# Kernel tuning notes

Measured on AMD Instinct MI355X. Metric: run time of the kernel, lower is better.

The kernel has to match this reference:

```python
import jax, jax.numpy as jnp
import numpy as np

LN_EPS = 1e-5


def setup_inputs() -> dict:
    key = jax.random.key(0)
    ks = jax.random.split(key, 6)
    B, S, D = 4, 4096, 2048
    Db = D // 4  # bottleneck_dim = n_embd // compression_ratio
    hidden = jax.random.normal(ks[0], (B, S, D), dtype=jnp.float32)
    # LayerNorm params (torch defaults: gamma=1, beta=0)
    ln_gamma = jnp.ones((D,), dtype=jnp.float32)
    ln_beta = jnp.zeros((D,), dtype=jnp.float32)
    # Linear weights, torch default init: U(-1/sqrt(fan_in), 1/sqrt(fan_in))
    bd_lim = 1.0 / np.sqrt(D)
    W_down = jax.random.uniform(ks[1], (D, Db), minval=-bd_lim, maxval=bd_lim, dtype=jnp.float32)
    b_down = jax.random.uniform(ks[2], (Db,), minval=-bd_lim, maxval=bd_lim, dtype=jnp.float32)
    bu_lim = 1.0 / np.sqrt(Db)
    W_up = jax.random.uniform(ks[3], (Db, D), minval=-bu_lim, maxval=bu_lim, dtype=jnp.float32)
    b_up = jax.random.uniform(ks[4], (D,), minval=-bu_lim, maxval=bu_lim, dtype=jnp.float32)
    alpha = jnp.array(0.01, dtype=jnp.float32)
    return {
        "hidden": hidden,
        "ln_gamma": ln_gamma,
        "ln_beta": ln_beta,
        "W_down": W_down,
        "b_down": b_down,
        "W_up": W_up,
        "b_up": b_up,
        "alpha": alpha,
        "layer_idx": 0,
    }


def reference(hidden, ln_gamma, ln_beta, W_down, b_down, W_up, b_up, alpha, layer_idx):
    # LayerNorm over last dim
    mu = jnp.mean(hidden, axis=-1, keepdims=True)
    var = jnp.mean(jnp.square(hidden - mu), axis=-1, keepdims=True)
    h_norm = (hidden - mu) * jax.lax.rsqrt(var + LN_EPS) * ln_gamma + ln_beta
    # down-proj -> SiLU -> up-proj   [b s d] @ [d k] -> [b s k] -> [b s d]
    z = jnp.einsum("bsd,dk->bsk", h_norm, W_down) + b_down
    z = jax.nn.silu(z)
    bottleneck_out = jnp.einsum("bsk,kd->bsd", z, W_up) + b_up
    # alpha-gated residual
    return hidden + alpha * (bottleneck_out - hidden)
```

## Files before the change

### kernel.cpp

```cpp
#include <hip/hip_runtime.h>

typedef __bf16 bf16x8 __attribute__((ext_vector_type(8)));
typedef __bf16 bf16x4 __attribute__((ext_vector_type(4)));
typedef float f32x4 __attribute__((ext_vector_type(4)));

#define S_BARRIER() asm volatile("s_barrier" ::: "memory")
#define WAITCNT_VM(n) asm volatile("s_waitcnt vmcnt(" #n ")" ::: "memory")
#define WAITCNT_LGKM0() asm volatile("s_waitcnt lgkmcnt(0)" ::: "memory")

__global__ __launch_bounds__(256) void prep_w_kernel(
    const float* __restrict__ Wd, __bf16* __restrict__ Wtd,
    const float* __restrict__ Wu, __bf16* __restrict__ Wtu,
    const float* __restrict__ g, const float* __restrict__ be,
    float* __restrict__ C1, float* __restrict__ C2b,
    int D, int Db) {
    const int ntile_d = (Db / 32) * (D / 32);
    __shared__ float t[32][33];
    const int c = threadIdx.x & 31, r0 = threadIdx.x >> 5;
    if ((int)blockIdx.x < ntile_d) {
        const int K = D, N = Db, tile = blockIdx.x;
        const int tn = tile % (N / 32), tk = tile / (N / 32);
        const int n0 = tn * 32, k0 = tk * 32;
#pragma unroll
        for (int r = r0; r < 32; r += 8)
            t[r][c] = Wd[(size_t)(k0 + r) * N + n0 + c];
        __syncthreads();
        const float gv = g[k0 + c];
        const float bv = be[k0 + c];
        float c1p[4], c2p[4];
#pragma unroll
        for (int u = 0; u < 4; ++u) {
            const int r = r0 + u * 8;
            const float wv = t[c][r];
            const __bf16 w16 = (__bf16)(gv * wv);
            Wtd[(size_t)(n0 + r) * K + k0 + c] = w16;
            c1p[u] = (float)w16;
            c2p[u] = bv * wv;
        }
#pragma unroll
        for (int o = 16; o > 0; o >>= 1)
#pragma unroll
            for (int u = 0; u < 4; ++u) {
                c1p[u] += __shfl_xor(c1p[u], o);
                c2p[u] += __shfl_xor(c2p[u], o);
            }
        if (c == 0)
#pragma unroll
            for (int u = 0; u < 4; ++u) {
                atomicAdd(&C1[n0 + r0 + u * 8], c1p[u]);
                atomicAdd(&C2b[n0 + r0 + u * 8], c2p[u]);
            }
    } else {
        const int K = Db, N = D, tile = blockIdx.x - ntile_d;
        const int tn = tile % (N / 32), tk = tile / (N / 32);
        const int n0 = tn * 32, k0 = tk * 32;
#pragma unroll
        for (int r = r0; r < 32; r += 8)
            t[r][c] = Wu[(size_t)(k0 + r) * N + n0 + c];
        __syncthreads();
#pragma unroll
        for (int r = r0; r < 32; r += 8)
            Wtu[(size_t)(n0 + r) * K + k0 + c] = (__bf16)t[c][r];
    }
}

__global__ __launch_bounds__(256, 4) void fused_ln_down(
    const float* __restrict__ X, const __bf16* __restrict__ Bt,
    const float* __restrict__ C1, const float* __restrict__ C2b,
    __bf16* __restrict__ Z, int M, int N, int K) {
    constexpr int BM = 64, BN = 128, BK = 32;
    constexpr int WM = 32, WN = 64, MI = 2, NJ = 4;
    __shared__ __align__(16) __bf16 Ads[BM * BK];
    __shared__ __align__(16) __bf16 Bds[2][BN * BK];
    __shared__ float sRow[BM], ssRow[BM];

    const int tid = threadIdx.x;
    const int wave = tid >> 6, lane = tid & 63;
    const int bn = blockIdx.x, bm = blockIdx.y;
    const int row0 = bm * BM, col0 = bn * BN;
    const int wr = wave >> 1, wc = wave & 1;

    f32x4 acc[MI][NJ] = {};

    const int lrow = lane >> 2;
    const int chunk = (lane & 3) ^ (lrow & 3);
    const int arow = wave * 16 + lrow;
    const float* Axr = X + (size_t)(row0 + arow) * K + chunk * 8;
    const __bf16* Bg = Bt + (size_t)col0 * K;
    const int lk = chunk * 8;

    const int c = lane & 15, q = lane >> 4;

    auto stageB = [&](int k0, int b) {
#pragma unroll
        for (int p = 0; p < 2; ++p) {
            const int r = wave * 32 + p * 16;
            __builtin_amdgcn_global_load_lds(
                (__attribute__((address_space(1))) void*)(Bg + (size_t)(r + lrow) * K + k0 + lk),
                (__attribute__((address_space(3))) void*)(&Bds[b][r * BK]),
                16, 0, 0);
        }
    };

    float s = 0.f, ss = 0.f;
    const int nk = K / BK;
    stageB(0, 0);
    float4 a0 = *(const float4*)(Axr);
    float4 a1 = *(const float4*)(Axr + 4);
    for (int it = 0; it < nk; ++it) {
        const int cur = it & 1;
        float4 n0, n1;
        if (it + 1 < nk) {
            stageB((it + 1) * BK, cur ^ 1);
            n0 = *(const float4*)(Axr + (it + 1) * BK);
            n1 = *(const float4*)(Axr + (it + 1) * BK + 4);
            WAITCNT_VM(4);
        } else {
            WAITCNT_VM(0);
        }
        s += a0.x + a0.y + a0.z + a0.w + a1.x + a1.y + a1.z + a1.w;
        ss += a0.x * a0.x + a0.y * a0.y + a0.z * a0.z + a0.w * a0.w +
              a1.x * a1.x + a1.y * a1.y + a1.z * a1.z + a1.w * a1.w;
        bf16x8 av;
        av[0] = (__bf16)a0.x; av[1] = (__bf16)a0.y;
        av[2] = (__bf16)a0.z; av[3] = (__bf16)a0.w;
        av[4] = (__bf16)a1.x; av[5] = (__bf16)a1.y;
        av[6] = (__bf16)a1.z; av[7] = (__bf16)a1.w;
        *(bf16x8*)(&Ads[arow * BK + (lane & 3) * 8]) = av;
        WAITCNT_LGKM0();
        S_BARRIER();

        bf16x8 afW[NJ], bfA[MI];
#pragma unroll
        for (int j = 0; j < NJ; ++j) {
            const int rl = wc * WN + j * 16 + c;
            afW[j] = *(const bf16x8*)(&Bds[cur][rl * BK + ((q ^ (c & 3)) * 8)]);
        }
#pragma unroll
        for (int i = 0; i < MI; ++i) {
            const int rl = wr * WM + i * 16 + c;
            bfA[i] = *(const bf16x8*)(&Ads[rl * BK + ((q ^ (c & 3)) * 8)]);
        }
#pragma unroll
        for (int i = 0; i < MI; ++i)
#pragma unroll
            for (int j = 0; j < NJ; ++j)
                acc[i][j] = __builtin_amdgcn_mfma_f32_16x16x32_bf16(afW[j], bfA[i],
                                                                    acc[i][j], 0, 0, 0);
        WAITCNT_LGKM0();
        S_BARRIER();
        a0 = n0; a1 = n1;
    }

    s += __shfl_xor(s, 1);  s += __shfl_xor(s, 2);
    ss += __shfl_xor(ss, 1); ss += __shfl_xor(ss, 2);
    if ((lane & 3) == 0) { sRow[arow] = s; ssRow[arow] = ss; }
    __syncthreads();

    const float rK = 1.f / (float)K;
#pragma unroll
    for (int i = 0; i < MI; ++i) {
        const int rl = wr * WM + i * 16 + c;
        const float mu = sRow[rl] * rK;
        const float var = ssRow[rl] * rK - mu * mu;
        const float rstd = rsqrtf(var + 1e-5f);
        const float mrs = mu * rstd;
        const int rowg = row0 + rl;
#pragma unroll
        for (int j = 0; j < NJ; ++j) {
            const int colb = col0 + wc * WN + j * 16 + q * 4;
            const float4 c1 = *(const float4*)(C1 + colb);
            const float4 c2 = *(const float4*)(C2b + colb);
            float v0 = rstd * acc[i][j][0] - mrs * c1.x + c2.x;
            float v1 = rstd * acc[i][j][1] - mrs * c1.y + c2.y;
            float v2 = rstd * acc[i][j][2] - mrs * c1.z + c2.z;
            float v3 = rstd * acc[i][j][3] - mrs * c1.w + c2.w;
            bf16x4 o;
            o[0] = (__bf16)(v0 / (1.f + __expf(-v0)));
            o[1] = (__bf16)(v1 / (1.f + __expf(-v1)));
            o[2] = (__bf16)(v2 / (1.f + __expf(-v2)));
            o[3] = (__bf16)(v3 / (1.f + __expf(-v3)));
            *(bf16x4*)(Z + (size_t)rowg * N + colb) = o;
        }
    }
}

template <int EPI, int BM, int BN, int MINW>
__global__ __launch_bounds__(256, MINW) void gemm_bt(
    const __bf16* __restrict__ A, const __bf16* __restrict__ Bt,
    const float* __restrict__ bias, const float* __restrict__ hid,
    const float* __restrict__ alpha_p, void* __restrict__ Cout,
    int M, int N, int K) {
    constexpr int BK = 32;
    constexpr int WM = BM / 2, WN = BN / 2;
    constexpr int MI = WM / 16, NJ = WN / 16;
    constexpr int GA = BM / 64, GB = BN / 64;
    constexpr int L = GA + GB;
    __shared__ __align__(16) __bf16 Ads[2][BM * BK];
    __shared__ __align__(16) __bf16 Bds[2][BN * BK];

    const int tid = threadIdx.x;
    const int wave = tid >> 6;
    const int lane = tid & 63;
    const int bn = blockIdx.x, bm = blockIdx.y;
    const int row0 = bm * BM, col0 = bn * BN;
    const int wr = wave >> 1, wc = wave & 1;

    f32x4 acc[MI][NJ] = {};

    const __bf16* Ag = A + (size_t)row0 * K;
    const __bf16* Bg = Bt + (size_t)col0 * K;
    const int lrow = lane >> 2;
    const int lk = ((lane & 3) ^ (lrow & 3)) * 8;

    const int c = lane & 15;
    const int q = lane >> 4;

    auto stage = [&](int k0, int b) {
#pragma unroll
        for (int p = 0; p < GA; ++p) {
            const int r = wave * (16 * GA) + p * 16;
            __builtin_amdgcn_global_load_lds(
                (__attribute__((address_space(1))) void*)(Ag + (size_t)(r + lrow) * K + k0 + lk),
                (__attribute__((address_space(3))) void*)(&Ads[b][r * BK]),
                16, 0, 0);
        }
#pragma unroll
        for (int p = 0; p < GB; ++p) {
            const int r = wave * (16 * GB) + p * 16;
            __builtin_amdgcn_global_load_lds(
                (__attribute__((address_space(1))) void*)(Bg + (size_t)(r + lrow) * K + k0 + lk),
                (__attribute__((address_space(3))) void*)(&Bds[b][r * BK]),
                16, 0, 0);
        }
    };

    const int nk = K / BK;
    stage(0, 0);
    for (int it = 0; it < nk; ++it) {
        const int cur = it & 1;
        if (it + 1 < nk) {
            stage((it + 1) * BK, cur ^ 1);
            if constexpr (L == 3) WAITCNT_VM(3); else WAITCNT_VM(4);
        } else {
            WAITCNT_VM(0);
        }
        S_BARRIER();

        bf16x8 afW[NJ], bfA[MI];
#pragma unroll
        for (int j = 0; j < NJ; ++j) {
            const int rl = wc * WN + j * 16 + c;
            afW[j] = *(const bf16x8*)(&Bds[cur][rl * BK + ((q ^ (c & 3)) * 8)]);
        }
#pragma unroll
        for (int i = 0; i < MI; ++i) {
            const int rl = wr * WM + i * 16 + c;
            bfA[i] = *(const bf16x8*)(&Ads[cur][rl * BK + ((q ^ (c & 3)) * 8)]);
        }
#pragma unroll
        for (int i = 0; i < MI; ++i)
#pragma unroll
            for (int j = 0; j < NJ; ++j)
                acc[i][j] = __builtin_amdgcn_mfma_f32_16x16x32_bf16(afW[j], bfA[i],
                                                                    acc[i][j], 0, 0, 0);
        WAITCNT_LGKM0();
        S_BARRIER();
    }

    float alpha = (EPI == 1) ? *alpha_p : 0.f;
#pragma unroll
    for (int i = 0; i < MI; ++i) {
        const int rowg = row0 + wr * WM + i * 16 + c;
        if (EPI == 0) {
#pragma unroll
            for (int j = 0; j < NJ; ++j) {
                const int colb = col0 + wc * WN + j * 16 + q * 4;
                const float4 bv = *(const float4*)(bias + colb);
                float v0 = acc[i][j][0] + bv.x;
                float v1 = acc[i][j][1] + bv.y;
                float v2 = acc[i][j][2] + bv.z;
                float v3 = acc[i][j][3] + bv.w;
                const size_t idx = (size_t)rowg * N + colb;
                bf16x4 o;
                o[0] = (__bf16)(v0 / (1.f + __expf(-v0)));
                o[1] = (__bf16)(v1 / (1.f + __expf(-v1)));
                o[2] = (__bf16)(v2 / (1.f + __expf(-v2)));
                o[3] = (__bf16)(v3 / (1.f + __expf(-v3)));
                *(bf16x4*)((__bf16*)Cout + idx) = o;
            }
        } else {
            float4 hv[NJ];
#pragma unroll
            for (int j = 0; j < NJ; ++j) {
                const int colb = col0 + wc * WN + j * 16 + q * 4;
                hv[j] = *(const float4*)(hid + (size_t)rowg * N + colb);
            }
#pragma unroll
            for (int j = 0; j < NJ; ++j) {
                const int colb = col0 + wc * WN + j * 16 + q * 4;
                const float4 bv = *(const float4*)(bias + colb);
                float v0 = acc[i][j][0] + bv.x;
                float v1 = acc[i][j][1] + bv.y;
                float v2 = acc[i][j][2] + bv.z;
                float v3 = acc[i][j][3] + bv.w;
                float4 o;
                o.x = hv[j].x + alpha * (v0 - hv[j].x);
                o.y = hv[j].y + alpha * (v1 - hv[j].y);
                o.z = hv[j].z + alpha * (v2 - hv[j].z);
                o.w = hv[j].w + alpha * (v3 - hv[j].w);
                *(float4*)((float*)Cout + (size_t)rowg * N + colb) = o;
            }
        }
    }
}

extern "C" void kernel_launch(void* const* d_in, const int* in_sizes, int n_in,
                              void* d_out, int out_size, void* d_ws, size_t ws_size,
                              hipStream_t stream) {
    const float* hidden = (const float*)d_in[0];
    const float* ln_gamma = (const float*)d_in[1];
    const float* ln_beta = (const float*)d_in[2];
    const float* W_down = (const float*)d_in[3];
    const float* b_down = (const float*)d_in[4];
    const float* W_up = (const float*)d_in[5];
    const float* b_up = (const float*)d_in[6];
    const float* alpha = (const float*)d_in[7];
    float* out = (float*)d_out;

    const int D = in_sizes[2];
    const int Db = in_sizes[4];
    const int M = in_sizes[0] / D;

    char* w = (char*)d_ws;
    __bf16* z = (__bf16*)w;   w += (size_t)M * Db * sizeof(__bf16);
    __bf16* Wtd = (__bf16*)w; w += (size_t)D * Db * sizeof(__bf16);
    __bf16* Wtu = (__bf16*)w; w += (size_t)Db * D * sizeof(__bf16);
    float* C1 = (float*)w;    w += Db * sizeof(float);
    float* C2b = (float*)w;   w += Db * sizeof(float);

    hipMemsetAsync(C1, 0, Db * sizeof(float), stream);
    hipMemcpyAsync(C2b, b_down, Db * sizeof(float), hipMemcpyDeviceToDevice, stream);

    const int ntiles = 2 * (D / 32) * (Db / 32);
    prep_w_kernel<<<ntiles, 256, 0, stream>>>(W_down, Wtd, W_up, Wtu,
                                              ln_gamma, ln_beta, C1, C2b, D, Db);

    fused_ln_down<<<dim3(Db / 128, M / 64), 256, 0, stream>>>(
        hidden, Wtd, C1, C2b, z, M, Db, D);

    gemm_bt<1, 128, 128, 4><<<dim3(D / 128, M / 128), 256, 0, stream>>>(
        z, Wtu, b_up, hidden, alpha, (void*)out, M, D, Db);
}
```

Measured before the change: 406.8 us.

## Deepen K tile to 64 in fused LN-down GEMM and add nontemporal memory ops

The fused LayerNorm+down-projection kernel now processes a 64-wide K slice per iteration, split into two 32-wide sub-buffers, so half as many barriers and loop iterations are needed and more loads are in flight per step. A-tile shared memory is double-buffered per sub-block, and the occupancy hint drops from 4 to 3 waves per SIMD to fit the larger LDS and register footprint. Streaming loads of hidden and stores of Z and the output use nontemporal builtins to reduce cache pollution. The cost is lower occupancy and more registers held for the prefetched A values.

```diff
diff --git a/kernel.cpp b/kernel.cpp
--- a/kernel.cpp
+++ b/kernel.cpp
@@ -64,14 +64,14 @@
     }
 }
 
-__global__ __launch_bounds__(256, 4) void fused_ln_down(
+__global__ __launch_bounds__(256, 3) void fused_ln_down(
     const float* __restrict__ X, const __bf16* __restrict__ Bt,
     const float* __restrict__ C1, const float* __restrict__ C2b,
     __bf16* __restrict__ Z, int M, int N, int K) {
-    constexpr int BM = 64, BN = 128, BK = 32;
+    constexpr int BM = 64, BN = 128, BK = 64;
     constexpr int WM = 32, WN = 64, MI = 2, NJ = 4;
-    __shared__ __align__(16) __bf16 Ads[BM * BK];
-    __shared__ __align__(16) __bf16 Bds[2][BN * BK];
+    __shared__ __align__(16) __bf16 Ads[2][BM * 32];
+    __shared__ __align__(16) __bf16 Bds[2][2][BN * 32];
     __shared__ float sRow[BM], ssRow[BM];
 
     const int tid = threadIdx.x;
@@ -95,61 +95,81 @@
 #pragma unroll
         for (int p = 0; p < 2; ++p) {
             const int r = wave * 32 + p * 16;
-            __builtin_amdgcn_global_load_lds(
-                (__attribute__((address_space(1))) void*)(Bg + (size_t)(r + lrow) * K + k0 + lk),
-                (__attribute__((address_space(3))) void*)(&Bds[b][r * BK]),
-                16, 0, 0);
+#pragma unroll
+            for (int kb = 0; kb < 2; ++kb) {
+                __builtin_amdgcn_global_load_lds(
+                    (__attribute__((address_space(1))) void*)(Bg + (size_t)(r + lrow) * K + k0 + kb * 32 + lk),
+                    (__attribute__((address_space(3))) void*)(&Bds[b][kb][r * 32]),
+                    16, 0, 0);
+            }
+        }
+    };
+
+    auto ldA = [&](int it, f32x4* d) {
+#pragma unroll
+        for (int kb = 0; kb < 2; ++kb) {
+            d[kb * 2] = __builtin_nontemporal_load((const f32x4*)(Axr + it * BK + kb * 32));
+            d[kb * 2 + 1] = __builtin_nontemporal_load((const f32x4*)(Axr + it * BK + kb * 32 + 4));
         }
     };
 
     float s = 0.f, ss = 0.f;
     const int nk = K / BK;
     stageB(0, 0);
-    float4 a0 = *(const float4*)(Axr);
-    float4 a1 = *(const float4*)(Axr + 4);
+    f32x4 a[4];
+    ldA(0, a);
     for (int it = 0; it < nk; ++it) {
         const int cur = it & 1;
-        float4 n0, n1;
+        f32x4 nx[4];
         if (it + 1 < nk) {
             stageB((it + 1) * BK, cur ^ 1);
-            n0 = *(const float4*)(Axr + (it + 1) * BK);
-            n1 = *(const float4*)(Axr + (it + 1) * BK + 4);
-            WAITCNT_VM(4);
+            ldA(it + 1, nx);
+            WAITCNT_VM(8);
         } else {
             WAITCNT_VM(0);
         }
-        s += a0.x + a0.y + a0.z + a0.w + a1.x + a1.y + a1.z + a1.w;
-        ss += a0.x * a0.x + a0.y * a0.y + a0.z * a0.z + a0.w * a0.w +
-              a1.x * a1.x + a1.y * a1.y + a1.z * a1.z + a1.w * a1.w;
-        bf16x8 av;
-        av[0] = (__bf16)a0.x; av[1] = (__bf16)a0.y;
-        av[2] = (__bf16)a0.z; av[3] = (__bf16)a0.w;
-        av[4] = (__bf16)a1.x; av[5] = (__bf16)a1.y;
-        av[6] = (__bf16)a1.z; av[7] = (__bf16)a1.w;
-        *(bf16x8*)(&Ads[arow * BK + (lane & 3) * 8]) = av;
+#pragma unroll
+        for (int kb = 0; kb < 2; ++kb) {
+            bf16x8 av;
+            av[0] = (__bf16)a[kb * 2][0]; av[1] = (__bf16)a[kb * 2][1];
+            av[2] = (__bf16)a[kb * 2][2]; av[3] = (__bf16)a[kb * 2][3];
+            av[4] = (__bf16)a[kb * 2 + 1][0]; av[5] = (__bf16)a[kb * 2 + 1][1];
+            av[6] = (__bf16)a[kb * 2 + 1][2]; av[7] = (__bf16)a[kb * 2 + 1][3];
+            *(bf16x8*)(&Ads[kb][arow * 32 + (lane & 3) * 8]) = av;
+        }
         WAITCNT_LGKM0();
         S_BARRIER();
 
-        bf16x8 afW[NJ], bfA[MI];
-#pragma unroll
-        for (int j = 0; j < NJ; ++j) {
-            const int rl = wc * WN + j * 16 + c;
-            afW[j] = *(const bf16x8*)(&Bds[cur][rl * BK + ((q ^ (c & 3)) * 8)]);
-        }
-#pragma unroll
-        for (int i = 0; i < MI; ++i) {
-            const int rl = wr * WM + i * 16 + c;
-            bfA[i] = *(const bf16x8*)(&Ads[rl * BK + ((q ^ (c & 3)) * 8)]);
-        }
-#pragma unroll
-        for (int i = 0; i < MI; ++i)
-#pragma unroll
-            for (int j = 0; j < NJ; ++j)
-                acc[i][j] = __builtin_amdgcn_mfma_f32_16x16x32_bf16(afW[j], bfA[i],
-                                                                    acc[i][j], 0, 0, 0);
+#pragma unroll
+        for (int kb = 0; kb < 2; ++kb) {
+            bf16x8 afW[NJ], bfA[MI];
+#pragma unroll
+            for (int j = 0; j < NJ; ++j) {
+                const int rl = wc * WN + j * 16 + c;
+                afW[j] = *(const bf16x8*)(&Bds[cur][kb][rl * 32 + ((q ^ (c & 3)) * 8)]);
+            }
+#pragma unroll
+            for (int i = 0; i < MI; ++i) {
+                const int rl = wr * WM + i * 16 + c;
+                bfA[i] = *(const bf16x8*)(&Ads[kb][rl * 32 + ((q ^ (c & 3)) * 8)]);
+            }
+#pragma unroll
+            for (int i = 0; i < MI; ++i)
+#pragma unroll
+                for (int j = 0; j < NJ; ++j)
+                    acc[i][j] = __builtin_amdgcn_mfma_f32_16x16x32_bf16(afW[j], bfA[i],
+                                                                        acc[i][j], 0, 0, 0);
+        }
+#pragma unroll
+        for (int u = 0; u < 4; ++u) {
+            s += a[u][0] + a[u][1] + a[u][2] + a[u][3];
+            ss += a[u][0] * a[u][0] + a[u][1] * a[u][1] +
+                  a[u][2] * a[u][2] + a[u][3] * a[u][3];
+        }
         WAITCNT_LGKM0();
         S_BARRIER();
-        a0 = n0; a1 = n1;
+#pragma unroll
+        for (int u = 0; u < 4; ++u) a[u] = nx[u];
     }
 
     s += __shfl_xor(s, 1);  s += __shfl_xor(s, 2);
@@ -169,18 +189,18 @@
 #pragma unroll
         for (int j = 0; j < NJ; ++j) {
             const int colb = col0 + wc * WN + j * 16 + q * 4;
-            const float4 c1 = *(const float4*)(C1 + colb);
-            const float4 c2 = *(const float4*)(C2b + colb);
-            float v0 = rstd * acc[i][j][0] - mrs * c1.x + c2.x;
-            float v1 = rstd * acc[i][j][1] - mrs * c1.y + c2.y;
-            float v2 = rstd * acc[i][j][2] - mrs * c1.z + c2.z;
-            float v3 = rstd * acc[i][j][3] - mrs * c1.w + c2.w;
+            const f32x4 c1 = *(const f32x4*)(C1 + colb);
+            const f32x4 c2 = *(const f32x4*)(C2b + colb);
+            float v0 = rstd * acc[i][j][0] - mrs * c1[0] + c2[0];
+            float v1 = rstd * acc[i][j][1] - mrs * c1[1] + c2[1];
+            float v2 = rstd * acc[i][j][2] - mrs * c1[2] + c2[2];
+            float v3 = rstd * acc[i][j][3] - mrs * c1[3] + c2[3];
             bf16x4 o;
             o[0] = (__bf16)(v0 / (1.f + __expf(-v0)));
             o[1] = (__bf16)(v1 / (1.f + __expf(-v1)));
             o[2] = (__bf16)(v2 / (1.f + __expf(-v2)));
             o[3] = (__bf16)(v3 / (1.f + __expf(-v3)));
-            *(bf16x4*)(Z + (size_t)rowg * N + colb) = o;
+            __builtin_nontemporal_store(o, (bf16x4*)(Z + (size_t)rowg * N + colb));
         }
     }
 }
@@ -276,40 +296,42 @@
 #pragma unroll
             for (int j = 0; j < NJ; ++j) {
                 const int colb = col0 + wc * WN + j * 16 + q * 4;
-                const float4 bv = *(const float4*)(bias + colb);
-                float v0 = acc[i][j][0] + bv.x;
-                float v1 = acc[i][j][1] + bv.y;
-                float v2 = acc[i][j][2] + bv.z;
-                float v3 = acc[i][j][3] + bv.w;
+                const f32x4 bv = *(const f32x4*)(bias + colb);
+                float v0 = acc[i][j][0] + bv[0];
+                float v1 = acc[i][j][1] + bv[1];
+                float v2 = acc[i][j][2] + bv[2];
+                float v3 = acc[i][j][3] + bv[3];
                 const size_t idx = (size_t)rowg * N + colb;
                 bf16x4 o;
                 o[0] = (__bf16)(v0 / (1.f + __expf(-v0)));
                 o[1] = (__bf16)(v1 / (1.f + __expf(-v1)));
                 o[2] = (__bf16)(v2 / (1.f + __expf(-v2)));
                 o[3] = (__bf16)(v3 / (1.f + __expf(-v3)));
-                *(bf16x4*)((__bf16*)Cout + idx) = o;
+                __builtin_nontemporal_store(o, (bf16x4*)((__bf16*)Cout + idx));
             }
         } else {
-            float4 hv[NJ];
+            f32x4 hv[NJ];
 #pragma unroll
             for (int j = 0; j < NJ; ++j) {
                 const int colb = col0 + wc * WN + j * 16 + q * 4;
-                hv[j] = *(const float4*)(hid + (size_t)rowg * N + colb);
+                hv[j] = __builtin_nontemporal_load(
+                    (const f32x4*)(hid + (size_t)rowg * N + colb));
             }
 #pragma unroll
             for (int j = 0; j < NJ; ++j) {
                 const int colb = col0 + wc * WN + j * 16 + q * 4;
-                const float4 bv = *(const float4*)(bias + colb);
-                float v0 = acc[i][j][0] + bv.x;
-                float v1 = acc[i][j][1] + bv.y;
-                float v2 = acc[i][j][2] + bv.z;
-                float v3 = acc[i][j][3] + bv.w;
-                float4 o;
-                o.x = hv[j].x + alpha * (v0 - hv[j].x);
-                o.y = hv[j].y + alpha * (v1 - hv[j].y);
-                o.z = hv[j].z + alpha * (v2 - hv[j].z);
-                o.w = hv[j].w + alpha * (v3 - hv[j].w);
-                *(float4*)((float*)Cout + (size_t)rowg * N + colb) = o;
+                const f32x4 bv = *(const f32x4*)(bias + colb);
+                float v0 = acc[i][j][0] + bv[0];
+                float v1 = acc[i][j][1] + bv[1];
+                float v2 = acc[i][j][2] + bv[2];
+                float v3 = acc[i][j][3] + bv[3];
+                f32x4 o;
+                o[0] = hv[j][0] + alpha * (v0 - hv[j][0]);
+                o[1] = hv[j][1] + alpha * (v1 - hv[j][1]);
+                o[2] = hv[j][2] + alpha * (v2 - hv[j][2]);
+                o[3] = hv[j][3] + alpha * (v3 - hv[j][3]);
+                __builtin_nontemporal_store(
+                    o, (f32x4*)((float*)Cout + (size_t)rowg * N + colb));
             }
         }
     }
@@ -339,8 +361,8 @@
     float* C1 = (float*)w;    w += Db * sizeof(float);
     float* C2b = (float*)w;   w += Db * sizeof(float);
 
-    hipMemsetAsync(C1, 0, Db * sizeof(float), stream);
-    hipMemcpyAsync(C2b, b_down, Db * sizeof(float), hipMemcpyDeviceToDevice, stream);
+    (void)hipMemsetAsync(C1, 0, Db * sizeof(float), stream);
+    (void)hipMemcpyAsync(C2b, b_down, Db * sizeof(float), hipMemcpyDeviceToDevice, stream);
 
     const int ntiles = 2 * (D / 32) * (Db / 32);
     prep_w_kernel<<<ntiles, 256, 0, stream>>>(W_down, Wtd, W_up, Wtu,
```

Result: slower. 476.7 us (+17.2%).

## Remap fused LN-down blocks per XCD and merge setup memset/memcpy

Applied to the files above, without the earlier changes.

The fused LayerNorm+down-projection kernel now uses a 1D grid and remaps block IDs so that each of the 8 XCDs handles a fixed column tile of W_down and a contiguous range of rows. The goal is better L2 reuse of weights and of hidden rows across the CU chiplets. The b_down bias is now added in the epilogue instead of being pre-copied into C2, so the device-to-device memcpy goes away and the two zeroing operations become one memset. Row-statistics accumulation is moved after the MFMA issue so it can overlap with matrix work. The remapping assumes round-robin dispatch of blocks to XCDs, and it falls back to the plain mapping when the shape does not divide evenly.

```diff
diff --git a/kernel.cpp b/kernel.cpp
--- a/kernel.cpp
+++ b/kernel.cpp
@@ -12,7 +12,7 @@
     const float* __restrict__ Wd, __bf16* __restrict__ Wtd,
     const float* __restrict__ Wu, __bf16* __restrict__ Wtu,
     const float* __restrict__ g, const float* __restrict__ be,
-    float* __restrict__ C1, float* __restrict__ C2b,
+    float* __restrict__ C1, float* __restrict__ C2w,
     int D, int Db) {
     const int ntile_d = (Db / 32) * (D / 32);
     __shared__ float t[32][33];
@@ -48,7 +48,7 @@
 #pragma unroll
             for (int u = 0; u < 4; ++u) {
                 atomicAdd(&C1[n0 + r0 + u * 8], c1p[u]);
-                atomicAdd(&C2b[n0 + r0 + u * 8], c2p[u]);
+                atomicAdd(&C2w[n0 + r0 + u * 8], c2p[u]);
             }
     } else {
         const int K = Db, N = D, tile = blockIdx.x - ntile_d;
@@ -66,7 +66,8 @@
 
 __global__ __launch_bounds__(256, 4) void fused_ln_down(
     const float* __restrict__ X, const __bf16* __restrict__ Bt,
-    const float* __restrict__ C1, const float* __restrict__ C2b,
+    const float* __restrict__ C1, const float* __restrict__ C2w,
+    const float* __restrict__ bd,
     __bf16* __restrict__ Z, int M, int N, int K) {
     constexpr int BM = 64, BN = 128, BK = 32;
     constexpr int WM = 32, WN = 64, MI = 2, NJ = 4;
@@ -76,7 +77,22 @@
 
     const int tid = threadIdx.x;
     const int wave = tid >> 6, lane = tid & 63;
-    const int bn = blockIdx.x, bm = blockIdx.y;
+
+    const int nbn = N / BN, nbm = M / BM;
+    int bn, bm;
+    {
+        const int id = blockIdx.x;
+        if (nbn <= 8 && (8 % nbn) == 0 && ((nbn * nbm) & 7) == 0 &&
+            (nbm % (8 / nbn)) == 0) {
+            const int per = 8 / nbn;
+            const int xcd = id & 7, slot = id >> 3;
+            bn = xcd / per;
+            bm = (xcd % per) * (nbm / per) + slot;
+        } else {
+            bn = id % nbn;
+            bm = id / nbn;
+        }
+    }
     const int row0 = bm * BM, col0 = bn * BN;
     const int wr = wave >> 1, wc = wave & 1;
 
@@ -105,27 +121,24 @@
     float s = 0.f, ss = 0.f;
     const int nk = K / BK;
     stageB(0, 0);
-    float4 a0 = *(const float4*)(Axr);
-    float4 a1 = *(const float4*)(Axr + 4);
+    f32x4 a0 = *(const f32x4*)(Axr);
+    f32x4 a1 = *(const f32x4*)(Axr + 4);
     for (int it = 0; it < nk; ++it) {
         const int cur = it & 1;
-        float4 n0, n1;
+        f32x4 n0, n1;
         if (it + 1 < nk) {
             stageB((it + 1) * BK, cur ^ 1);
-            n0 = *(const float4*)(Axr + (it + 1) * BK);
-            n1 = *(const float4*)(Axr + (it + 1) * BK + 4);
+            n0 = *(const f32x4*)(Axr + (it + 1) * BK);
+            n1 = *(const f32x4*)(Axr + (it + 1) * BK + 4);
             WAITCNT_VM(4);
         } else {
             WAITCNT_VM(0);
         }
-        s += a0.x + a0.y + a0.z + a0.w + a1.x + a1.y + a1.z + a1.w;
-        ss += a0.x * a0.x + a0.y * a0.y + a0.z * a0.z + a0.w * a0.w +
-              a1.x * a1.x + a1.y * a1.y + a1.z * a1.z + a1.w * a1.w;
         bf16x8 av;
-        av[0] = (__bf16)a0.x; av[1] = (__bf16)a0.y;
-        av[2] = (__bf16)a0.z; av[3] = (__bf16)a0.w;
-        av[4] = (__bf16)a1.x; av[5] = (__bf16)a1.y;
-        av[6] = (__bf16)a1.z; av[7] = (__bf16)a1.w;
+        av[0] = (__bf16)a0[0]; av[1] = (__bf16)a0[1];
+        av[2] = (__bf16)a0[2]; av[3] = (__bf16)a0[3];
+        av[4] = (__bf16)a1[0]; av[5] = (__bf16)a1[1];
+        av[6] = (__bf16)a1[2]; av[7] = (__bf16)a1[3];
         *(bf16x8*)(&Ads[arow * BK + (lane & 3) * 8]) = av;
         WAITCNT_LGKM0();
         S_BARRIER();
@@ -147,6 +160,9 @@
             for (int j = 0; j < NJ; ++j)
                 acc[i][j] = __builtin_amdgcn_mfma_f32_16x16x32_bf16(afW[j], bfA[i],
                                                                     acc[i][j], 0, 0, 0);
+        s += a0[0] + a0[1] + a0[2] + a0[3] + a1[0] + a1[1] + a1[2] + a1[3];
+        ss += a0[0] * a0[0] + a0[1] * a0[1] + a0[2] * a0[2] + a0[3] * a0[3] +
+              a1[0] * a1[0] + a1[1] * a1[1] + a1[2] * a1[2] + a1[3] * a1[3];
         WAITCNT_LGKM0();
         S_BARRIER();
         a0 = n0; a1 = n1;
@@ -169,12 +185,13 @@
 #pragma unroll
         for (int j = 0; j < NJ; ++j) {
             const int colb = col0 + wc * WN + j * 16 + q * 4;
-            const float4 c1 = *(const float4*)(C1 + colb);
-            const float4 c2 = *(const float4*)(C2b + colb);
-            float v0 = rstd * acc[i][j][0] - mrs * c1.x + c2.x;
-            float v1 = rstd * acc[i][j][1] - mrs * c1.y + c2.y;
-            float v2 = rstd * acc[i][j][2] - mrs * c1.z + c2.z;
-            float v3 = rstd * acc[i][j][3] - mrs * c1.w + c2.w;
+            const f32x4 c1 = *(const f32x4*)(C1 + colb);
+            const f32x4 c2 = *(const f32x4*)(C2w + colb);
+            const f32x4 bb = *(const f32x4*)(bd + colb);
+            float v0 = rstd * acc[i][j][0] - mrs * c1[0] + c2[0] + bb[0];
+            float v1 = rstd * acc[i][j][1] - mrs * c1[1] + c2[1] + bb[1];
+            float v2 = rstd * acc[i][j][2] - mrs * c1[2] + c2[2] + bb[2];
+            float v3 = rstd * acc[i][j][3] - mrs * c1[3] + c2[3] + bb[3];
             bf16x4 o;
             o[0] = (__bf16)(v0 / (1.f + __expf(-v0)));
             o[1] = (__bf16)(v1 / (1.f + __expf(-v1)));
@@ -276,11 +293,11 @@
 #pragma unroll
             for (int j = 0; j < NJ; ++j) {
                 const int colb = col0 + wc * WN + j * 16 + q * 4;
-                const float4 bv = *(const float4*)(bias + colb);
-                float v0 = acc[i][j][0] + bv.x;
-                float v1 = acc[i][j][1] + bv.y;
-                float v2 = acc[i][j][2] + bv.z;
-                float v3 = acc[i][j][3] + bv.w;
+                const f32x4 bv = *(const f32x4*)(bias + colb);
+                float v0 = acc[i][j][0] + bv[0];
+                float v1 = acc[i][j][1] + bv[1];
+                float v2 = acc[i][j][2] + bv[2];
+                float v3 = acc[i][j][3] + bv[3];
                 const size_t idx = (size_t)rowg * N + colb;
                 bf16x4 o;
                 o[0] = (__bf16)(v0 / (1.f + __expf(-v0)));
@@ -290,26 +307,26 @@
                 *(bf16x4*)((__bf16*)Cout + idx) = o;
             }
         } else {
-            float4 hv[NJ];
+            f32x4 hv[NJ];
 #pragma unroll
             for (int j = 0; j < NJ; ++j) {
                 const int colb = col0 + wc * WN + j * 16 + q * 4;
-                hv[j] = *(const float4*)(hid + (size_t)rowg * N + colb);
+                hv[j] = *(const f32x4*)(hid + (size_t)rowg * N + colb);
             }
 #pragma unroll
             for (int j = 0; j < NJ; ++j) {
                 const int colb = col0 + wc * WN + j * 16 + q * 4;
-                const float4 bv = *(const float4*)(bias + colb);
-                float v0 = acc[i][j][0] + bv.x;
-                float v1 = acc[i][j][1] + bv.y;
-                float v2 = acc[i][j][2] + bv.z;
-                float v3 = acc[i][j][3] + bv.w;
-                float4 o;
-                o.x = hv[j].x + alpha * (v0 - hv[j].x);
-                o.y = hv[j].y + alpha * (v1 - hv[j].y);
-                o.z = hv[j].z + alpha * (v2 - hv[j].z);
-                o.w = hv[j].w + alpha * (v3 - hv[j].w);
-                *(float4*)((float*)Cout + (size_t)rowg * N + colb) = o;
+                const f32x4 bv = *(const f32x4*)(bias + colb);
+                float v0 = acc[i][j][0] + bv[0];
+                float v1 = acc[i][j][1] + bv[1];
+                float v2 = acc[i][j][2] + bv[2];
+                float v3 = acc[i][j][3] + bv[3];
+                f32x4 o;
+                o[0] = hv[j][0] + alpha * (v0 - hv[j][0]);
+                o[1] = hv[j][1] + alpha * (v1 - hv[j][1]);
+                o[2] = hv[j][2] + alpha * (v2 - hv[j][2]);
+                o[3] = hv[j][3] + alpha * (v3 - hv[j][3]);
+                *(f32x4*)((float*)Cout + (size_t)rowg * N + colb) = o;
             }
         }
     }
@@ -337,17 +354,16 @@
     __bf16* Wtd = (__bf16*)w; w += (size_t)D * Db * sizeof(__bf16);
     __bf16* Wtu = (__bf16*)w; w += (size_t)Db * D * sizeof(__bf16);
     float* C1 = (float*)w;    w += Db * sizeof(float);
-    float* C2b = (float*)w;   w += Db * sizeof(float);
-
-    hipMemsetAsync(C1, 0, Db * sizeof(float), stream);
-    hipMemcpyAsync(C2b, b_down, Db * sizeof(float), hipMemcpyDeviceToDevice, stream);
+    float* C2w = (float*)w;   w += Db * sizeof(float);
+
+    (void)hipMemsetAsync(C1, 0, 2 * Db * sizeof(float), stream);
 
     const int ntiles = 2 * (D / 32) * (Db / 32);
     prep_w_kernel<<<ntiles, 256, 0, stream>>>(W_down, Wtd, W_up, Wtu,
-                                              ln_gamma, ln_beta, C1, C2b, D, Db);
-
-    fused_ln_down<<<dim3(Db / 128, M / 64), 256, 0, stream>>>(
-        hidden, Wtd, C1, C2b, z, M, Db, D);
+                                              ln_gamma, ln_beta, C1, C2w, D, Db);
+
+    fused_ln_down<<<(M / 64) * (Db / 128), 256, 0, stream>>>(
+        hidden, Wtd, C1, C2w, b_down, z, M, Db, D);
 
     gemm_bt<1, 128, 128, 4><<<dim3(D / 128, M / 128), 256, 0, stream>>>(
         z, Wtu, b_up, hidden, alpha, (void*)out, M, D, Db);
```

New measurement: 411.4 us. Within noise of the previous version (+1.1%).
